# Kernel optimization log

Hardware: AMD Instinct MI355X
Metric: run time of the kernel (lower is better)

The kernel has to match this reference:

```python
import jax, jax.numpy as jnp
import numpy as np

N = 32768   # total nodes
P = 1024    # nodes per graph
B = 32      # graphs (N = B*P)
D = 256     # dim_h
H = 8       # num_heads
E = 262144  # edges
BN_EPS = 1e-5


def setup_inputs() -> dict:
    key = jax.random.key(0)
    ks = jax.random.split(key, 24)
    s = 0.05
    x = jax.random.normal(ks[0], (N, D), jnp.float32)
    src = jax.random.randint(ks[1], (E,), 0, N, dtype=jnp.int32)
    dst = (src // P) * P + jax.random.randint(ks[2], (E,), 0, P, dtype=jnp.int32)
    edge_index = jnp.stack([src, dst])  # [2, E], edges within the same graph
    edge_attr = jax.random.normal(ks[3], (E, D), jnp.float32)
    return {
        "x": x,
        "edge_index": edge_index,
        "edge_attr": edge_attr,
        # GINE nn: Linear(D,D) -> ReLU -> Linear(D,D)
        "gin_w1": s * jax.random.normal(ks[4], (D, D)),
        "gin_b1": jnp.zeros((D,)),
        "gin_w2": s * jax.random.normal(ks[5], (D, D)),
        "gin_b2": jnp.zeros((D,)),
        # MultiheadAttention packed in-proj and out-proj
        "in_w": s * jax.random.normal(ks[6], (3 * D, D)),
        "in_b": jnp.zeros((3 * D,)),
        "out_w": s * jax.random.normal(ks[7], (D, D)),
        "out_b": jnp.zeros((D,)),
        # BatchNorm1d affine params (training-mode batch stats)
        "bn1l_g": jnp.ones((D,)) + s * jax.random.normal(ks[8], (D,)),
        "bn1l_b": s * jax.random.normal(ks[9], (D,)),
        "bn1a_g": jnp.ones((D,)) + s * jax.random.normal(ks[10], (D,)),
        "bn1a_b": s * jax.random.normal(ks[11], (D,)),
        # FF block: Linear(D,2D) -> ReLU -> Linear(2D,D)
        "ff_w1": s * jax.random.normal(ks[12], (2 * D, D)),
        "ff_b1": jnp.zeros((2 * D,)),
        "ff_w2": s * jax.random.normal(ks[13], (D, 2 * D)),
        "ff_b2": jnp.zeros((D,)),
        "bn2_g": jnp.ones((D,)) + s * jax.random.normal(ks[14], (D,)),
        "bn2_b": s * jax.random.normal(ks[15], (D,)),
    }


def _batchnorm(x, g, b):
    # BatchNorm1d, training mode: biased batch statistics over the node axis.
    m = jnp.mean(x, axis=0)
    v = jnp.mean((x - m) ** 2, axis=0)
    return g * (x - m) * jax.lax.rsqrt(v + BN_EPS) + b


def reference(x, edge_index, edge_attr, gin_w1, gin_b1, gin_w2, gin_b2,
              in_w, in_b, out_w, out_b, bn1l_g, bn1l_b, bn1a_g, bn1a_b,
              ff_w1, ff_b1, ff_w2, ff_b2, bn2_g, bn2_b):
    h_in = x
    # ---- local branch: GINEConv (eps = 0) ----
    msg = jax.nn.relu(x[edge_index[0]] + edge_attr)          # [E, D]
    aggr = jax.ops.segment_sum(msg, edge_index[1], num_segments=N)
    z = x + aggr                                             # (1+eps)*x_i + sum msg
    h_local = jax.nn.relu(z @ gin_w1.T + gin_b1) @ gin_w2.T + gin_b2
    h_local = _batchnorm(h_in + h_local, bn1l_g, bn1l_b)
    # ---- global branch: dense-batch MHA (equal-size graphs -> full mask) ----
    hd = x.reshape(B, P, D)
    qkv = hd @ in_w.T + in_b                                 # [B, P, 3D]
    q, k, v = jnp.split(qkv, 3, axis=-1)
    dh = D // H
    q = q.reshape(B, P, H, dh).transpose(0, 2, 1, 3)         # [B, H, P, dh]
    k = k.reshape(B, P, H, dh).transpose(0, 2, 1, 3)
    v = v.reshape(B, P, H, dh).transpose(0, 2, 1, 3)
    scores = jnp.einsum("bhqd,bhkd->bhqk", q, k) / np.sqrt(dh)
    attn = jax.nn.softmax(scores, axis=-1)
    o = jnp.einsum("bhqk,bhkd->bhqd", attn, v)               # [B, H, P, dh]
    o = o.transpose(0, 2, 1, 3).reshape(B, P, D) @ out_w.T + out_b
    h_attn = o.reshape(N, D)
    h_attn = _batchnorm(h_in + h_attn, bn1a_g, bn1a_b)
    # ---- combine + FF + norm ----
    h = h_local + h_attn
    ff = jax.nn.relu(h @ ff_w1.T + ff_b1) @ ff_w2.T + ff_b2
    h = _batchnorm(h + ff, bn2_g, bn2_b)
    return h
```

## Files before the change

kernel.cpp:

```cpp
#include <hip/hip_runtime.h>
#include <hip/hip_bf16.h>

constexpr int D = 256;
constexpr int PG = 1024;
constexpr int BSLOT = 64;

typedef __attribute__((ext_vector_type(8))) short bf16x8;
typedef __attribute__((ext_vector_type(4))) float f32x4;

__device__ inline short f2bf(float f) {
    __hip_bfloat16 h = __float2bfloat16(f);
    return *reinterpret_cast<short*>(&h);
}
__device__ inline float bf2f(short s) {
    return __uint_as_float(((unsigned)(unsigned short)s) << 16);
}

__global__ __launch_bounds__(256) void prep_kernel(
    const float* __restrict__ w1, const float* __restrict__ w2,
    const float* __restrict__ w3, const float* __restrict__ w4,
    const float* __restrict__ w5, const float* __restrict__ w6,
    short* __restrict__ out,
    const int* __restrict__ src, const int* __restrict__ dst,
    int* __restrict__ cnt, int2* __restrict__ bucket, int E)
{
    int bid = blockIdx.x;
    if (bid >= 320) {
        int e = (bid - 320) * 256 + threadIdx.x;
        if (e < E) {
            int d = dst[e];
            int pos = atomicAdd(&cnt[d], 1);
            if (pos < BSLOT) {
                int2 v; v.x = e; v.y = src[e];
                bucket[d * BSLOT + pos] = v;
            }
        }
        return;
    }
    int i = bid * 256 + threadIdx.x;
    const float* sp; int base;
    if (i < 16384)      { if (i < 8192) { sp = w1; base = 0; }
                          else          { sp = w2; base = 8192; } }
    else if (i < 40960) { sp = w3; base = 16384; }
    else if (i < 49152) { sp = w4; base = 40960; }
    else if (i < 65536) { sp = w5; base = 49152; }
    else                { sp = w6; base = 65536; }
    int k = i - base;
    float4 a = ((const float4*)sp)[k * 2];
    float4 b = ((const float4*)sp)[k * 2 + 1];
    bf16x8 v;
    v[0] = f2bf(a.x); v[1] = f2bf(a.y); v[2] = f2bf(a.z); v[3] = f2bf(a.w);
    v[4] = f2bf(b.x); v[5] = f2bf(b.y); v[6] = f2bf(b.z); v[7] = f2bf(b.w);
    ((bf16x8*)out)[i] = v;
}

__global__ __launch_bounds__(256) void csr_aggr(
    const float* __restrict__ x, const float* __restrict__ ea,
    const int* __restrict__ cnt, const int2* __restrict__ bucket,
    short* __restrict__ z, short* __restrict__ xb)
{
    int gid = blockIdx.x * 256 + threadIdx.x;
    int node = gid >> 6;
    int c = (gid & 63) << 2;
    int deg = cnt[node];
    if (deg > BSLOT) deg = BSLOT;
    const int2* bk = bucket + (size_t)node * BSLOT;
    float4 xv = *(const float4*)(x + (size_t)node * D + c);
    short4 xr;
    xr.x = f2bf(xv.x); xr.y = f2bf(xv.y); xr.z = f2bf(xv.z); xr.w = f2bf(xv.w);
    *(short4*)(xb + (size_t)node * D + c) = xr;
    float4 acc = xv;
    for (int i = 0; i < deg; ++i) {
        int2 es = bk[i];
        float4 xa = *(const float4*)(x + (size_t)es.y * D + c);
        float4 av = *(const float4*)(ea + (size_t)es.x * D + c);
        acc.x += fmaxf(xa.x + av.x, 0.f);
        acc.y += fmaxf(xa.y + av.y, 0.f);
        acc.z += fmaxf(xa.z + av.z, 0.f);
        acc.w += fmaxf(xa.w + av.w, 0.f);
    }
    short4 r;
    r.x = f2bf(acc.x); r.y = f2bf(acc.y); r.z = f2bf(acc.z); r.w = f2bf(acc.w);
    *(short4*)(z + (size_t)node * D + c) = r;
}

template<bool RELU, bool ADDB, bool STATS, bool SCALEQ>
__device__ __forceinline__ void gemm_body(
    int bid, int nbx, int nwg,
    const short* __restrict__ X, const short* __restrict__ W,
    const float* __restrict__ bias, const short* __restrict__ addb,
    short* __restrict__ Y, float* __restrict__ st, int K, int M,
    short* SM)
{
    short* Xs = SM;
    short* Ws = SM + 9216;

    const int cpx = nwg >> 3;
    const int wg  = (bid & 7) * cpx + (bid >> 3);
    const int r0 = (wg / nbx) * 128;
    const int c0 = (wg % nbx) * 128;

    const int t = threadIdx.x, w = t >> 6, l = t & 63;
    const int wr = w >> 1, wc = w & 1, lg = l >> 4, lm = l & 15;
    const int srow = t >> 3;
    const int scol = (t & 7) * 8;

    f32x4 acc[4][4];
    #pragma unroll
    for (int i = 0; i < 4; ++i)
        #pragma unroll
        for (int j = 0; j < 4; ++j)
            acc[i][j] = (f32x4){0.f, 0.f, 0.f, 0.f};

    for (int k0 = 0; k0 < K; k0 += 64) {
        __syncthreads();
        #pragma unroll
        for (int it = 0; it < 4; ++it) {
            int r = it * 32 + srow;
            bf16x8 xv = *(const bf16x8*)(X + (size_t)(r0 + r) * K + k0 + scol);
            bf16x8 wv = *(const bf16x8*)(W + (size_t)(c0 + r) * K + k0 + scol);
            *(bf16x8*)&Xs[r * 72 + scol] = xv;
            *(bf16x8*)&Ws[r * 72 + scol] = wv;
        }
        __syncthreads();

        bf16x8 af[4][2], bfr[4][2];
        #pragma unroll
        for (int i = 0; i < 4; ++i)
            #pragma unroll
            for (int ks = 0; ks < 2; ++ks) {
                af[i][ks]  = *(const bf16x8*)&Xs[(wr*64 + i*16 + lm)*72 + ks*32 + lg*8];
                bfr[i][ks] = *(const bf16x8*)&Ws[(wc*64 + i*16 + lm)*72 + ks*32 + lg*8];
            }
        #pragma unroll
        for (int i = 0; i < 4; ++i)
            #pragma unroll
            for (int j = 0; j < 4; ++j) {
                acc[i][j] = __builtin_amdgcn_mfma_f32_16x16x32_bf16(af[i][0], bfr[j][0], acc[i][j], 0, 0, 0);
                acc[i][j] = __builtin_amdgcn_mfma_f32_16x16x32_bf16(af[i][1], bfr[j][1], acc[i][j], 0, 0, 0);
            }
    }

    float s4[4] = {}, q4[4] = {};
    #pragma unroll
    for (int j = 0; j < 4; ++j) {
        int col = c0 + wc*64 + j*16 + lm;
        float bj = bias[col];
        #pragma unroll
        for (int i = 0; i < 4; ++i) {
            #pragma unroll
            for (int r = 0; r < 4; ++r) {
                int row = r0 + wr*64 + i*16 + lg*4 + r;
                size_t off = (size_t)row * M + col;
                float v = acc[i][j][r] + bj;
                if (RELU) v = fmaxf(v, 0.f);
                if (SCALEQ) { if (col < 256) v *= 0.17677669529663687f; }
                if (ADDB) v += bf2f(addb[off]);
                if (STATS) { s4[j] += v; q4[j] = fmaf(v, v, q4[j]); }
                Y[off] = f2bf(v);
            }
        }
    }
    if (STATS) {
        #pragma unroll
        for (int j = 0; j < 4; ++j) {
            s4[j] += __shfl_xor(s4[j], 16); q4[j] += __shfl_xor(q4[j], 16);
            s4[j] += __shfl_xor(s4[j], 32); q4[j] += __shfl_xor(q4[j], 32);
        }
        if (lg == 0) {
            #pragma unroll
            for (int j = 0; j < 4; ++j) {
                int col = c0 + wc*64 + j*16 + lm;
                atomicAdd(&st[col], s4[j]);
                atomicAdd(&st[256 + col], q4[j]);
            }
        }
    }
}

template<bool RELU, bool ADDB, bool STATS, bool SCALEQ>
__global__ __launch_bounds__(256) void gemm_k(
    const short* __restrict__ X, const short* __restrict__ W,
    const float* __restrict__ bias, const short* __restrict__ addb,
    short* __restrict__ Y, float* __restrict__ st, int K, int M, int nbx)
{
    __shared__ __align__(16) short SM[18432];
    gemm_body<RELU, ADDB, STATS, SCALEQ>(
        blockIdx.x, nbx, gridDim.x, X, W, bias, addb, Y, st, K, M, SM);
}

__global__ __launch_bounds__(256) void gemm_dual(
    const short* __restrict__ X1, const short* __restrict__ W1,
    const float* __restrict__ b1, const short* __restrict__ add1,
    short* __restrict__ Y1, float* __restrict__ st1,
    const short* __restrict__ X2, const short* __restrict__ W2,
    const float* __restrict__ b2, const short* __restrict__ add2,
    short* __restrict__ Y2, float* __restrict__ st2)
{
    __shared__ __align__(16) short SM[18432];
    int bid = blockIdx.x;
    if (bid & 1)
        gemm_body<false, true, true, false>(
            bid >> 1, 2, 512, X2, W2, b2, add2, Y2, st2, 256, 256, SM);
    else
        gemm_body<false, true, true, false>(
            bid >> 1, 2, 512, X1, W1, b1, add1, Y1, st1, 256, 256, SM);
}

__global__ __launch_bounds__(256) void attn_mfma(
    const short* __restrict__ QKV, short* __restrict__ O)
{
    const int bh = blockIdx.x & 255;
    const int qblk = blockIdx.x >> 8;
    const int b = bh >> 3, h = bh & 7;
    const int t = threadIdx.x, w = t >> 6, l = t & 63;
    const int lg = l >> 4, lm = l & 15;
    const size_t gb = (size_t)b * PG * 768;
    const int q0 = qblk * 256 + w * 64;

    __shared__ __align__(16) short Ks[64 * 40];
    __shared__ __align__(16) short Vt[32 * 72];
    __shared__ __align__(16) short Ps[4][32 * 72];

    bf16x8 qa[4];
    #pragma unroll
    for (int qt = 0; qt < 4; ++qt)
        qa[qt] = *(const bf16x8*)(QKV + gb + (size_t)(q0 + qt*16 + lm) * 768 + h*32 + lg*8);

    f32x4 acc[4][2];
    #pragma unroll
    for (int qt = 0; qt < 4; ++qt)
        #pragma unroll
        for (int hf = 0; hf < 2; ++hf)
            acc[qt][hf] = (f32x4){0.f, 0.f, 0.f, 0.f};
    float lsum[4] = {0.f, 0.f, 0.f, 0.f};

    const int srow = t >> 2;
    const int sq = (t & 3) * 8;
    const short* Kb = QKV + gb + 256 + h*32 + sq;
    const short* Vb = QKV + gb + 512 + h*32 + sq;

    bf16x8 kreg = *(const bf16x8*)(Kb + (size_t)srow * 768);
    bf16x8 vreg = *(const bf16x8*)(Vb + (size_t)srow * 768);

    for (int kt = 0; kt < 16; ++kt) {
        *(bf16x8*)&Ks[srow * 40 + sq] = kreg;
        #pragma unroll
        for (int j = 0; j < 8; ++j) Vt[(sq + j) * 72 + srow] = vreg[j];
        __syncthreads();
        if (kt < 15) {
            kreg = *(const bf16x8*)(Kb + (size_t)((kt + 1) * 64 + srow) * 768);
            vreg = *(const bf16x8*)(Vb + (size_t)((kt + 1) * 64 + srow) * 768);
        }

        bf16x8 kf[4];
        #pragma unroll
        for (int s = 0; s < 4; ++s)
            kf[s] = *(const bf16x8*)&Ks[(s*16 + lm) * 40 + lg*8];

        bf16x8 vf[2][2];
        #pragma unroll
        for (int hf = 0; hf < 2; ++hf)
            #pragma unroll
            for (int g = 0; g < 2; ++g)
                vf[hf][g] = *(const bf16x8*)&Vt[(hf*16 + lm) * 72 + g*32 + lg*8];

        #pragma unroll
        for (int h2 = 0; h2 < 2; ++h2) {
            #pragma unroll
            for (int qi = 0; qi < 2; ++qi) {
                const int qt = h2 * 2 + qi;
                #pragma unroll
                for (int s = 0; s < 4; ++s) {
                    f32x4 c = (f32x4){0.f, 0.f, 0.f, 0.f};
                    c = __builtin_amdgcn_mfma_f32_16x16x32_bf16(kf[s], qa[qt], c, 0, 0, 0);
                    float p0 = __expf(c[0]), p1 = __expf(c[1]);
                    float p2 = __expf(c[2]), p3 = __expf(c[3]);
                    lsum[qt] += (p0 + p1) + (p2 + p3);
                    short4 pk;
                    pk.x = f2bf(p0); pk.y = f2bf(p1); pk.z = f2bf(p2); pk.w = f2bf(p3);
                    *(short4*)&Ps[w][(qi*16 + lm) * 72 + s*16 + lg*4] = pk;
                }
            }
            #pragma unroll
            for (int qi = 0; qi < 2; ++qi) {
                const int qt = h2 * 2 + qi;
                #pragma unroll
                for (int g = 0; g < 2; ++g) {
                    bf16x8 pf = *(const bf16x8*)&Ps[w][(qi*16 + lm) * 72 + g*32 + lg*8];
                    #pragma unroll
                    for (int hf = 0; hf < 2; ++hf)
                        acc[qt][hf] = __builtin_amdgcn_mfma_f32_16x16x32_bf16(
                            pf, vf[hf][g], acc[qt][hf], 0, 0, 0);
                }
            }
        }
        __syncthreads();
    }

    float red[4];
    #pragma unroll
    for (int qt = 0; qt < 4; ++qt) {
        float v = lsum[qt];
        v += __shfl_xor(v, 16);
        v += __shfl_xor(v, 32);
        red[qt] = 1.0f / v;
    }
    #pragma unroll
    for (int qt = 0; qt < 4; ++qt) {
        #pragma unroll
        for (int r = 0; r < 4; ++r) {
            float inv = __shfl(red[qt], lg*4 + r);
            int qrow = q0 + qt*16 + lg*4 + r;
            short* Op = O + ((size_t)b * PG + qrow) * D + h * 32;
            Op[lm]      = f2bf(acc[qt][0][r] * inv);
            Op[16 + lm] = f2bf(acc[qt][1][r] * inv);
        }
    }
}

__global__ __launch_bounds__(256) void bn_combine(
    const short* __restrict__ A, const short* __restrict__ Bq,
    const float* __restrict__ gl, const float* __restrict__ bl,
    const float* __restrict__ ga, const float* __restrict__ ba,
    const float* __restrict__ st, short* __restrict__ H, int n)
{
    const float invN = 1.0f / (float)n;
    size_t i = (size_t)blockIdx.x * 256 + threadIdx.x;
    int c0 = (int)((i & 31) << 3);
    bf16x8 av = ((const bf16x8*)A)[i];
    bf16x8 bv = ((const bf16x8*)Bq)[i];
    bf16x8 o;
    #pragma unroll
    for (int e = 0; e < 8; ++e) {
        int c = c0 + e;
        float m1 = st[c] * invN;
        float v1 = fmaxf(st[256 + c] * invN - m1 * m1, 0.f);
        float m2 = st[512 + c] * invN;
        float v2 = fmaxf(st[768 + c] * invN - m2 * m2, 0.f);
        float y1 = gl[c] * (bf2f(av[e]) - m1) * rsqrtf(v1 + 1e-5f) + bl[c];
        float y2 = ga[c] * (bf2f(bv[e]) - m2) * rsqrtf(v2 + 1e-5f) + ba[c];
        o[e] = f2bf(y1 + y2);
    }
    ((bf16x8*)H)[i] = o;
}

__global__ __launch_bounds__(256) void bn_apply(
    const short* __restrict__ X, const float* __restrict__ g,
    const float* __restrict__ bb, const float* __restrict__ st,
    float* __restrict__ out, int n)
{
    const float invN = 1.0f / (float)n;
    size_t i = (size_t)blockIdx.x * 256 + threadIdx.x;
    int c0 = (int)((i & 31) << 3);
    bf16x8 xv = ((const bf16x8*)X)[i];
    float r[8];
    #pragma unroll
    for (int e = 0; e < 8; ++e) {
        int c = c0 + e;
        float m = st[c] * invN;
        float v = fmaxf(st[256 + c] * invN - m * m, 0.f);
        r[e] = g[c] * (bf2f(xv[e]) - m) * rsqrtf(v + 1e-5f) + bb[c];
    }
    float4 o0 = {r[0], r[1], r[2], r[3]};
    float4 o1 = {r[4], r[5], r[6], r[7]};
    ((float4*)out)[i * 2]     = o0;
    ((float4*)out)[i * 2 + 1] = o1;
}

extern "C" void kernel_launch(void* const* d_in, const int* in_sizes, int n_in,
                              void* d_out, int out_size, void* d_ws, size_t ws_size,
                              hipStream_t stream)
{
    const float* x    = (const float*)d_in[0];
    const int*   ei   = (const int*)d_in[1];
    const float* ea   = (const float*)d_in[2];
    const float* gw1  = (const float*)d_in[3];
    const float* gb1  = (const float*)d_in[4];
    const float* gw2  = (const float*)d_in[5];
    const float* gb2  = (const float*)d_in[6];
    const float* inw  = (const float*)d_in[7];
    const float* inb  = (const float*)d_in[8];
    const float* outw = (const float*)d_in[9];
    const float* outb = (const float*)d_in[10];
    const float* g1l  = (const float*)d_in[11];
    const float* b1l  = (const float*)d_in[12];
    const float* g1a  = (const float*)d_in[13];
    const float* b1a  = (const float*)d_in[14];
    const float* fw1  = (const float*)d_in[15];
    const float* fb1  = (const float*)d_in[16];
    const float* fw2  = (const float*)d_in[17];
    const float* fb2  = (const float*)d_in[18];
    const float* g2   = (const float*)d_in[19];
    const float* b2   = (const float*)d_in[20];
    float* out = (float*)d_out;

    const int N = in_sizes[0] / D;
    const int E = in_sizes[1] / 2;
    const size_t ND = (size_t)N * D;

    short* Bp = (short*)d_ws;
    short* S0 = Bp;
    short* S1 = Bp + ND;
    short* S2 = Bp + 2 * ND;
    short* S3 = Bp + 3 * ND;
    short* S4 = Bp + 4 * ND;
    short* S5 = Bp + 5 * ND;
    short* xb = Bp + 6 * ND;
    short* Wb = Bp + 7 * ND;
    short* gw1b = Wb, *gw2b = Wb + 65536, *inwb = Wb + 131072;
    short* outwb = Wb + 327680, *fw1b = Wb + 393216, *fw2b = Wb + 524288;
    float* st = (float*)(Wb + 655360);
    int* cnt = (int*)(st + 1536);
    int2* bucket = (int2*)(cnt + N);

    const int EB = (E + 255) / 256;

    hipMemsetAsync(st, 0, (1536 + (size_t)N) * sizeof(int), stream);
    prep_kernel<<<320 + EB, 256, 0, stream>>>(
        gw1, gw2, inw, outw, fw1, fw2, Wb, ei, ei + E, cnt, bucket, E);

    csr_aggr<<<(N * 64) / 256, 256, 0, stream>>>(x, ea, cnt, bucket, S0, xb);

    gemm_k<true , false, false, false><<<512, 256, 0, stream>>>(
        S0, gw1b, gb1, nullptr, S5, nullptr, 256, 256, 2);

    gemm_k<false, false, false, true ><<<1536, 256, 0, stream>>>(
        xb, inwb, inb, nullptr, S0, nullptr, 256, 768, 6);

    attn_mfma<<<(N / PG) * 8 * 4, 256, 0, stream>>>(S0, S4);

    gemm_dual<<<1024, 256, 0, stream>>>(
        S5, gw2b, gb2, xb, S3, st,
        S4, outwb, outb, xb, S0, st + 512);

    bn_combine<<<(unsigned)(ND / 8 / 256), 256, 0, stream>>>(
        S3, S0, g1l, b1l, g1a, b1a, st, S1, N);
    gemm_k<true , false, false, false><<<1024, 256, 0, stream>>>(
        S1, fw1b, fb1, nullptr, S2, nullptr, 256, 512, 4);
    gemm_k<false, true , true , false><<<512, 256, 0, stream>>>(
        S2, fw2b, fb2, S1, S4, st + 1024, 512, 256, 2);
    bn_apply<<<(unsigned)(ND / 8 / 256), 256, 0, stream>>>(
        S4, g2, b2, st + 1024, out, N);
}
```

Baseline: 338.1 us.

## Fuse GIN-W1 and QKV GEMMs, fold Q scale into weights, transpose epilogue stores

Merges the GIN first-layer GEMM and the QKV in-projection GEMM into one launch that interleaves their tiles, with the attention scale folded into the bf16 in-proj weights and a pre-scaled bias computed in the prep kernel. A TRANS mode swaps the MFMA operands so each lane holds four consecutive output columns, which allows vectorized short4 stores and float4 bias loads in the epilogue for the non-stats GEMMs. The aim is to cut one launch and tail, and to replace scattered 2-byte stores with wider ones. It adds an extra workspace buffer and a runtime relu flag, and rounding changes slightly because Q is scaled before the bf16 conversion.

```diff
diff --git a/kernel.cpp b/kernel.cpp
--- a/kernel.cpp
+++ b/kernel.cpp
@@ -20,11 +20,21 @@
     const float* __restrict__ w1, const float* __restrict__ w2,
     const float* __restrict__ w3, const float* __restrict__ w4,
     const float* __restrict__ w5, const float* __restrict__ w6,
-    short* __restrict__ out,
+    short* __restrict__ out, const float* __restrict__ inb,
+    float* __restrict__ ibs,
     const int* __restrict__ src, const int* __restrict__ dst,
-    int* __restrict__ cnt, int2* __restrict__ bucket, int E)
-{
+    int* __restrict__ cnt, int2* __restrict__ bucket, int E, int EB)
+{
+    const float rs = 0.17677669529663687f;
     int bid = blockIdx.x;
+    if (bid >= 320 + EB) {
+        #pragma unroll
+        for (int r = 0; r < 3; ++r) {
+            int i = r * 256 + threadIdx.x;
+            ibs[i] = inb[i] * (i < 256 ? rs : 1.0f);
+        }
+        return;
+    }
     if (bid >= 320) {
         int e = (bid - 320) * 256 + threadIdx.x;
         if (e < E) {
@@ -38,10 +48,11 @@
         return;
     }
     int i = bid * 256 + threadIdx.x;
-    const float* sp; int base;
+    const float* sp; int base; float sc = 1.0f;
     if (i < 16384)      { if (i < 8192) { sp = w1; base = 0; }
                           else          { sp = w2; base = 8192; } }
-    else if (i < 40960) { sp = w3; base = 16384; }
+    else if (i < 40960) { sp = w3; base = 16384;
+                          if (i - 16384 < 8192) sc = rs; }
     else if (i < 49152) { sp = w4; base = 40960; }
     else if (i < 65536) { sp = w5; base = 49152; }
     else                { sp = w6; base = 65536; }
@@ -49,8 +60,8 @@
     float4 a = ((const float4*)sp)[k * 2];
     float4 b = ((const float4*)sp)[k * 2 + 1];
     bf16x8 v;
-    v[0] = f2bf(a.x); v[1] = f2bf(a.y); v[2] = f2bf(a.z); v[3] = f2bf(a.w);
-    v[4] = f2bf(b.x); v[5] = f2bf(b.y); v[6] = f2bf(b.z); v[7] = f2bf(b.w);
+    v[0] = f2bf(a.x * sc); v[1] = f2bf(a.y * sc); v[2] = f2bf(a.z * sc); v[3] = f2bf(a.w * sc);
+    v[4] = f2bf(b.x * sc); v[5] = f2bf(b.y * sc); v[6] = f2bf(b.z * sc); v[7] = f2bf(b.w * sc);
     ((bf16x8*)out)[i] = v;
 }
 
@@ -84,9 +95,9 @@
     *(short4*)(z + (size_t)node * D + c) = r;
 }
 
-template<bool RELU, bool ADDB, bool STATS, bool SCALEQ>
+template<bool TRANS, bool ADDB, bool STATS>
 __device__ __forceinline__ void gemm_body(
-    int bid, int nbx, int nwg,
+    int bid, int nbx, int nwg, bool relu,
     const short* __restrict__ X, const short* __restrict__ W,
     const float* __restrict__ bias, const short* __restrict__ addb,
     short* __restrict__ Y, float* __restrict__ st, int K, int M,
@@ -136,57 +147,116 @@
         for (int i = 0; i < 4; ++i)
             #pragma unroll
             for (int j = 0; j < 4; ++j) {
-                acc[i][j] = __builtin_amdgcn_mfma_f32_16x16x32_bf16(af[i][0], bfr[j][0], acc[i][j], 0, 0, 0);
-                acc[i][j] = __builtin_amdgcn_mfma_f32_16x16x32_bf16(af[i][1], bfr[j][1], acc[i][j], 0, 0, 0);
-            }
-    }
-
-    float s4[4] = {}, q4[4] = {};
-    #pragma unroll
-    for (int j = 0; j < 4; ++j) {
-        int col = c0 + wc*64 + j*16 + lm;
-        float bj = bias[col];
+                if (TRANS) {
+                    acc[i][j] = __builtin_amdgcn_mfma_f32_16x16x32_bf16(bfr[j][0], af[i][0], acc[i][j], 0, 0, 0);
+                    acc[i][j] = __builtin_amdgcn_mfma_f32_16x16x32_bf16(bfr[j][1], af[i][1], acc[i][j], 0, 0, 0);
+                } else {
+                    acc[i][j] = __builtin_amdgcn_mfma_f32_16x16x32_bf16(af[i][0], bfr[j][0], acc[i][j], 0, 0, 0);
+                    acc[i][j] = __builtin_amdgcn_mfma_f32_16x16x32_bf16(af[i][1], bfr[j][1], acc[i][j], 0, 0, 0);
+                }
+            }
+    }
+
+    if (TRANS) {
         #pragma unroll
         for (int i = 0; i < 4; ++i) {
-            #pragma unroll
-            for (int r = 0; r < 4; ++r) {
-                int row = r0 + wr*64 + i*16 + lg*4 + r;
-                size_t off = (size_t)row * M + col;
-                float v = acc[i][j][r] + bj;
-                if (RELU) v = fmaxf(v, 0.f);
-                if (SCALEQ) { if (col < 256) v *= 0.17677669529663687f; }
-                if (ADDB) v += bf2f(addb[off]);
-                if (STATS) { s4[j] += v; q4[j] = fmaf(v, v, q4[j]); }
-                Y[off] = f2bf(v);
-            }
-        }
-    }
-    if (STATS) {
+            int row = r0 + wr*64 + i*16 + lm;
+            #pragma unroll
+            for (int j = 0; j < 4; ++j) {
+                int col0 = c0 + wc*64 + j*16 + lg*4;
+                float4 bj = *(const float4*)(bias + col0);
+                size_t off = (size_t)row * M + col0;
+                float v0 = acc[i][j][0] + bj.x;
+                float v1 = acc[i][j][1] + bj.y;
+                float v2 = acc[i][j][2] + bj.z;
+                float v3 = acc[i][j][3] + bj.w;
+                if (relu) {
+                    v0 = fmaxf(v0, 0.f); v1 = fmaxf(v1, 0.f);
+                    v2 = fmaxf(v2, 0.f); v3 = fmaxf(v3, 0.f);
+                }
+                if (ADDB) {
+                    short4 ab = *(const short4*)(addb + off);
+                    v0 += bf2f(ab.x); v1 += bf2f(ab.y);
+                    v2 += bf2f(ab.z); v3 += bf2f(ab.w);
+                }
+                short4 o;
+                o.x = f2bf(v0); o.y = f2bf(v1); o.z = f2bf(v2); o.w = f2bf(v3);
+                *(short4*)(Y + off) = o;
+            }
+        }
+    } else {
+        float s4[4] = {}, q4[4] = {};
         #pragma unroll
         for (int j = 0; j < 4; ++j) {
-            s4[j] += __shfl_xor(s4[j], 16); q4[j] += __shfl_xor(q4[j], 16);
-            s4[j] += __shfl_xor(s4[j], 32); q4[j] += __shfl_xor(q4[j], 32);
-        }
-        if (lg == 0) {
+            int col = c0 + wc*64 + j*16 + lm;
+            float bj = bias[col];
+            #pragma unroll
+            for (int i = 0; i < 4; ++i) {
+                #pragma unroll
+                for (int r = 0; r < 4; ++r) {
+                    int row = r0 + wr*64 + i*16 + lg*4 + r;
+                    size_t off = (size_t)row * M + col;
+                    float v = acc[i][j][r] + bj;
+                    if (relu) v = fmaxf(v, 0.f);
+                    if (ADDB) v += bf2f(addb[off]);
+                    if (STATS) { s4[j] += v; q4[j] = fmaf(v, v, q4[j]); }
+                    Y[off] = f2bf(v);
+                }
+            }
+        }
+        if (STATS) {
             #pragma unroll
             for (int j = 0; j < 4; ++j) {
-                int col = c0 + wc*64 + j*16 + lm;
-                atomicAdd(&st[col], s4[j]);
-                atomicAdd(&st[256 + col], q4[j]);
-            }
-        }
-    }
-}
-
-template<bool RELU, bool ADDB, bool STATS, bool SCALEQ>
-__global__ __launch_bounds__(256) void gemm_k(
+                s4[j] += __shfl_xor(s4[j], 16); q4[j] += __shfl_xor(q4[j], 16);
+                s4[j] += __shfl_xor(s4[j], 32); q4[j] += __shfl_xor(q4[j], 32);
+            }
+            if (lg == 0) {
+                #pragma unroll
+                for (int j = 0; j < 4; ++j) {
+                    int col = c0 + wc*64 + j*16 + lm;
+                    atomicAdd(&st[col], s4[j]);
+                    atomicAdd(&st[256 + col], q4[j]);
+                }
+            }
+        }
+    }
+}
+
+__global__ __launch_bounds__(256) void gemm_ab(
+    const short* __restrict__ Zb, const short* __restrict__ gw1b,
+    const float* __restrict__ gb1, short* __restrict__ T1b,
+    const short* __restrict__ xb, const short* __restrict__ inwb,
+    const float* __restrict__ ibs, short* __restrict__ QKVb)
+{
+    __shared__ __align__(16) short SM[18432];
+    int bid = blockIdx.x;
+    int grp = bid >> 2, rem = bid & 3;
+    if (rem == 0)
+        gemm_body<true, false, false>(
+            grp, 2, 512, true, Zb, gw1b, gb1, nullptr, T1b, nullptr, 256, 256, SM);
+    else
+        gemm_body<true, false, false>(
+            grp * 3 + rem - 1, 6, 1536, false, xb, inwb, ibs, nullptr, QKVb, nullptr, 256, 768, SM);
+}
+
+__global__ __launch_bounds__(256) void gemm_t(
+    const short* __restrict__ X, const short* __restrict__ W,
+    const float* __restrict__ bias, short* __restrict__ Y,
+    int K, int M, int nbx)
+{
+    __shared__ __align__(16) short SM[18432];
+    gemm_body<true, false, false>(
+        blockIdx.x, nbx, gridDim.x, true, X, W, bias, nullptr, Y, nullptr, K, M, SM);
+}
+
+__global__ __launch_bounds__(256) void gemm_s(
     const short* __restrict__ X, const short* __restrict__ W,
     const float* __restrict__ bias, const short* __restrict__ addb,
     short* __restrict__ Y, float* __restrict__ st, int K, int M, int nbx)
 {
     __shared__ __align__(16) short SM[18432];
-    gemm_body<RELU, ADDB, STATS, SCALEQ>(
-        blockIdx.x, nbx, gridDim.x, X, W, bias, addb, Y, st, K, M, SM);
+    gemm_body<false, true, true>(
+        blockIdx.x, nbx, gridDim.x, false, X, W, bias, addb, Y, st, K, M, SM);
 }
 
 __global__ __launch_bounds__(256) void gemm_dual(
@@ -200,11 +270,11 @@
     __shared__ __align__(16) short SM[18432];
     int bid = blockIdx.x;
     if (bid & 1)
-        gemm_body<false, true, true, false>(
-            bid >> 1, 2, 512, X2, W2, b2, add2, Y2, st2, 256, 256, SM);
+        gemm_body<false, true, true>(
+            bid >> 1, 2, 512, false, X2, W2, b2, add2, Y2, st2, 256, 256, SM);
     else
-        gemm_body<false, true, true, false>(
-            bid >> 1, 2, 512, X1, W1, b1, add1, Y1, st1, 256, 256, SM);
+        gemm_body<false, true, true>(
+            bid >> 1, 2, 512, false, X1, W1, b1, add1, Y1, st1, 256, 256, SM);
 }
 
 __global__ __launch_bounds__(256) void attn_mfma(
@@ -406,27 +476,25 @@
     short* S3 = Bp + 3 * ND;
     short* S4 = Bp + 4 * ND;
     short* S5 = Bp + 5 * ND;
-    short* xb = Bp + 6 * ND;
-    short* Wb = Bp + 7 * ND;
+    short* S6 = Bp + 6 * ND;
+    short* xb = Bp + 7 * ND;
+    short* Wb = Bp + 8 * ND;
     short* gw1b = Wb, *gw2b = Wb + 65536, *inwb = Wb + 131072;
     short* outwb = Wb + 327680, *fw1b = Wb + 393216, *fw2b = Wb + 524288;
     float* st = (float*)(Wb + 655360);
     int* cnt = (int*)(st + 1536);
-    int2* bucket = (int2*)(cnt + N);
+    float* ibs = (float*)(cnt + N);
+    int2* bucket = (int2*)(ibs + 768);
 
     const int EB = (E + 255) / 256;
 
     hipMemsetAsync(st, 0, (1536 + (size_t)N) * sizeof(int), stream);
-    prep_kernel<<<320 + EB, 256, 0, stream>>>(
-        gw1, gw2, inw, outw, fw1, fw2, Wb, ei, ei + E, cnt, bucket, E);
-
-    csr_aggr<<<(N * 64) / 256, 256, 0, stream>>>(x, ea, cnt, bucket, S0, xb);
-
-    gemm_k<true , false, false, false><<<512, 256, 0, stream>>>(
-        S0, gw1b, gb1, nullptr, S5, nullptr, 256, 256, 2);
-
-    gemm_k<false, false, false, true ><<<1536, 256, 0, stream>>>(
-        xb, inwb, inb, nullptr, S0, nullptr, 256, 768, 6);
+    prep_kernel<<<320 + EB + 1, 256, 0, stream>>>(
+        gw1, gw2, inw, outw, fw1, fw2, Wb, inb, ibs, ei, ei + E, cnt, bucket, E, EB);
+
+    csr_aggr<<<(N * 64) / 256, 256, 0, stream>>>(x, ea, cnt, bucket, S6, xb);
+
+    gemm_ab<<<2048, 256, 0, stream>>>(S6, gw1b, gb1, S5, xb, inwb, ibs, S0);
 
     attn_mfma<<<(N / PG) * 8 * 4, 256, 0, stream>>>(S0, S4);
 
@@ -436,10 +504,8 @@
 
     bn_combine<<<(unsigned)(ND / 8 / 256), 256, 0, stream>>>(
         S3, S0, g1l, b1l, g1a, b1a, st, S1, N);
-    gemm_k<true , false, false, false><<<1024, 256, 0, stream>>>(
-        S1, fw1b, fb1, nullptr, S2, nullptr, 256, 512, 4);
-    gemm_k<false, true , true , false><<<512, 256, 0, stream>>>(
-        S2, fw2b, fb2, S1, S4, st + 1024, 512, 256, 2);
+    gemm_t<<<1024, 256, 0, stream>>>(S1, fw1b, fb1, S2, 256, 512, 4);
+    gemm_s<<<512, 256, 0, stream>>>(S2, fw2b, fb2, S1, S4, st + 1024, 512, 256, 2);
     bn_apply<<<(unsigned)(ND / 8 / 256), 256, 0, stream>>>(
         S4, g2, b2, st + 1024, out, N);
 }
```

After: 363.4 us. 1.07x slower.
